# Optimization experiments

Hardware: AMD Instinct MI355X
Metric: run time of the kernel (lower is better)

The kernel has to match this reference:

```python
import jax, jax.numpy as jnp
import numpy as np

B, CL, QL, D = 32, 1024, 256, 768


def masked_softmax(x, m, axis):
    # Faithful port of the torch helper: clamp, pre-mask, stable exp, post-mask, eps-normalize.
    x = jnp.clip(x, -15.0, 15.0)
    x = x * m
    e_x = jnp.exp(x - jnp.max(x, axis=axis, keepdims=True))
    e_x = e_x * m
    return e_x / (jnp.sum(e_x, axis=axis, keepdims=True) + 1e-6)


def setup_inputs() -> dict:
    key = jax.random.key(0)
    k1, k2, k3, k4, k5 = jax.random.split(key, 5)
    C = jax.random.normal(k1, (B, CL, D), dtype=jnp.float32)
    Q = jax.random.normal(k2, (B, QL, D), dtype=jnp.float32)
    w = jax.random.normal(k3, (3 * D,), dtype=jnp.float32) * 0.02  # xavier-scale
    c_mask = jax.random.randint(k4, (B, CL), 0, 2, dtype=jnp.int32)
    q_mask = jax.random.randint(k5, (B, QL), 0, 2, dtype=jnp.int32)
    return {"C": C, "Q": Q, "w": w, "c_mask": c_mask, "q_mask": q_mask}


def reference(C, Q, w, c_mask, q_mask):
    d = C.shape[-1]
    w1, w2, w3 = w[:d], w[d:2 * d], w[2 * d:]
    # Trilinear decomposition of cat([C,Q,C*Q]) @ w -- same math, no [b,c,q,3d] blowup.
    S = (jnp.einsum('bid,d->bi', C, w1)[:, :, None]
         + jnp.einsum('bjd,d->bj', Q, w2)[:, None, :]
         + jnp.einsum('bid,bjd->bij', C * w3, Q))  # [B, CL, QL]
    qm = q_mask.astype(jnp.float32)[:, None, :]  # [B,1,QL]
    cm = c_mask.astype(jnp.float32)[:, :, None]  # [B,CL,1]
    S1 = masked_softmax(S, qm, axis=2)
    A = jnp.einsum('bij,bjd->bid', S1, Q)  # [B, CL, D]
    S2 = masked_softmax(S, cm, axis=1)
    S2_max = jnp.max(S2, axis=1, keepdims=True)  # [B, 1, QL]
    Bmat = jnp.einsum('bij,bjd->bid', S2_max, Q)  # [B, 1, D], broadcast over CL
    Bmat = jnp.broadcast_to(Bmat, C.shape)
    return jnp.concatenate([C, A, C * A, C * Bmat], axis=-1)  # [B, CL, 4D]
```

## Files before the change

### kernel.cpp

```cpp
#include <hip/hip_runtime.h>

#define B_  32
#define CL_ 1024
#define QL_ 256
#define D_  768

typedef _Float16 f16x8 __attribute__((ext_vector_type(8)));
typedef float    f32x4 __attribute__((ext_vector_type(4)));

__global__ void rowdot_kernel(const float* __restrict__ X, const float* __restrict__ w,
                              float* __restrict__ out) {
    int wave = threadIdx.x >> 6;
    int lane = threadIdx.x & 63;
    int row  = blockIdx.x * 4 + wave;
    const float* x = X + (size_t)row * D_;
    float s = 0.f;
#pragma unroll
    for (int k = 0; k < D_ / 64; ++k) s += x[lane + k * 64] * w[lane + k * 64];
#pragma unroll
    for (int m = 32; m; m >>= 1) s += __shfl_xor(s, m, 64);
    if (lane == 0) out[row] = s;
}

__global__ __launch_bounds__(256) void prep_q_kernel(const float* __restrict__ Q,
                                                     _Float16* __restrict__ QT,
                                                     _Float16* __restrict__ Qh) {
    __shared__ float tile[64][65];
    int b  = blockIdx.z;
    int j0 = blockIdx.x * 64;
    int d0 = blockIdx.y * 64;
    int t  = threadIdx.x;
    int jj = t >> 4;
    int dd = (t & 15) * 4;
#pragma unroll
    for (int p = 0; p < 4; ++p) {
        int j = jj + p * 16;
        f32x4 v = *(const f32x4*)(Q + ((size_t)b * QL_ + j0 + j) * D_ + d0 + dd);
        *(f32x4*)&tile[j][dd] = v;
        _Float16 h[4] = {(_Float16)v[0], (_Float16)v[1], (_Float16)v[2], (_Float16)v[3]};
        *(uint2*)(Qh + ((size_t)b * QL_ + j0 + j) * D_ + d0 + dd) = *(uint2*)h;
    }
    __syncthreads();
    int j4 = (t & 15) * 4;
#pragma unroll
    for (int p = 0; p < 4; ++p) {
        int d = jj + p * 16;
        _Float16 h[4];
#pragma unroll
        for (int e = 0; e < 4; ++e) h[e] = (_Float16)tile[j4 + e][d];
        *(uint2*)(QT + ((size_t)b * D_ + d0 + d) * QL_ + j0 + j4) = *(uint2*)h;
    }
}

__global__ __launch_bounds__(512, 2) void fused_s_kernel(
    const float* __restrict__ C, const _Float16* __restrict__ Qh,
    const float* __restrict__ w, const float* __restrict__ qw2g,
    const int* __restrict__ c_mask, const int* __restrict__ q_mask,
    _Float16* __restrict__ S1h, float* __restrict__ pmg,
    float* __restrict__ psg, float* __restrict__ pumg) {
    __shared__ __align__(16) _Float16 As[128 * 64];
    __shared__ __align__(16) _Float16 Bs[256 * 64];
    __shared__ float w1s[D_], w3s[D_];
    __shared__ float cw1s[128];
    __shared__ float rowredM[512], rowredS[512];
    __shared__ int   cms[128], qms[256];

    int t = threadIdx.x;
    int bid = blockIdx.x;
    int b = bid & 31;
    int slice = bid >> 5;
    int i0 = slice * 128;
    int wave = t >> 6, lane = t & 63, lrow = lane & 15, lk = lane >> 4;
    int wr = wave >> 2, wc = wave & 3;
    int jw = wc * 64;

    for (int k = t; k < D_; k += 512) { w1s[k] = w[k]; w3s[k] = w[2 * D_ + k]; }
    if (t < 128) cms[t] = c_mask[b * CL_ + i0 + t];
    if (t < 256) qms[t] = q_mask[b * QL_ + t];

    const float* Cbase = C + ((size_t)b * CL_ + i0) * D_;
    const _Float16* Qbase = Qh + (size_t)b * QL_ * D_;

    f32x4 acc[4][4] = {};
    float cwp0 = 0.f, cwp1 = 0.f;
    int arow0 = t >> 3, arow1 = 64 + (t >> 3);
    int asc = t & 7;

    for (int k0 = 0; k0 < D_; k0 += 64) {
        __syncthreads();
        {
            int kk0 = k0 + asc * 8;
            float4 w30 = *(const float4*)(&w3s[kk0]);
            float4 w31 = *(const float4*)(&w3s[kk0 + 4]);
            float4 w10 = *(const float4*)(&w1s[kk0]);
            float4 w11 = *(const float4*)(&w1s[kk0 + 4]);
            const float* src0 = Cbase + (size_t)arow0 * D_ + kk0;
            float4 a0 = *(const float4*)src0;
            float4 a1 = *(const float4*)(src0 + 4);
            f16x8 ah;
            ah[0] = (_Float16)(a0.x * w30.x); ah[1] = (_Float16)(a0.y * w30.y);
            ah[2] = (_Float16)(a0.z * w30.z); ah[3] = (_Float16)(a0.w * w30.w);
            ah[4] = (_Float16)(a1.x * w31.x); ah[5] = (_Float16)(a1.y * w31.y);
            ah[6] = (_Float16)(a1.z * w31.z); ah[7] = (_Float16)(a1.w * w31.w);
            cwp0 += a0.x * w10.x + a0.y * w10.y + a0.z * w10.z + a0.w * w10.w
                  + a1.x * w11.x + a1.y * w11.y + a1.z * w11.z + a1.w * w11.w;
            *(f16x8*)&As[arow0 * 64 + ((asc ^ (arow0 & 7)) * 8)] = ah;
            const float* src1 = Cbase + (size_t)arow1 * D_ + kk0;
            float4 b0 = *(const float4*)src1;
            float4 b1 = *(const float4*)(src1 + 4);
            f16x8 bh;
            bh[0] = (_Float16)(b0.x * w30.x); bh[1] = (_Float16)(b0.y * w30.y);
            bh[2] = (_Float16)(b0.z * w30.z); bh[3] = (_Float16)(b0.w * w30.w);
            bh[4] = (_Float16)(b1.x * w31.x); bh[5] = (_Float16)(b1.y * w31.y);
            bh[6] = (_Float16)(b1.z * w31.z); bh[7] = (_Float16)(b1.w * w31.w);
            cwp1 += b0.x * w10.x + b0.y * w10.y + b0.z * w10.z + b0.w * w10.w
                  + b1.x * w11.x + b1.y * w11.y + b1.z * w11.z + b1.w * w11.w;
            *(f16x8*)&As[arow1 * 64 + ((asc ^ (arow1 & 7)) * 8)] = bh;
        }
#pragma unroll
        for (int sb = 0; sb < 4; ++sb) {
            int row = sb * 64 + (t >> 3);
            f16x8 bh = *(const f16x8*)(Qbase + (size_t)row * D_ + k0 + asc * 8);
            *(f16x8*)&Bs[row * 64 + ((asc ^ (row & 7)) * 8)] = bh;
        }
        __syncthreads();
#pragma unroll
        for (int kk = 0; kk < 2; ++kk) {
            int slot = kk * 4 + lk;
            int swa = (slot ^ (lrow & 7)) * 8;
            f16x8 af[4];
#pragma unroll
            for (int m = 0; m < 4; ++m)
                af[m] = *(const f16x8*)&As[(wr * 64 + m * 16 + lrow) * 64 + swa];
#pragma unroll
            for (int n = 0; n < 4; ++n) {
                int rb = jw + n * 16 + lrow;
                f16x8 bf = *(const f16x8*)&Bs[rb * 64 + swa];
#pragma unroll
                for (int m = 0; m < 4; ++m)
                    acc[m][n] = __builtin_amdgcn_mfma_f32_16x16x32_f16(af[m], bf, acc[m][n], 0, 0, 0);
            }
        }
    }

    cwp0 += __shfl_xor(cwp0, 1, 64); cwp0 += __shfl_xor(cwp0, 2, 64); cwp0 += __shfl_xor(cwp0, 4, 64);
    cwp1 += __shfl_xor(cwp1, 1, 64); cwp1 += __shfl_xor(cwp1, 2, 64); cwp1 += __shfl_xor(cwp1, 4, 64);
    if ((t & 7) == 0) { cw1s[arow0] = cwp0; cw1s[arow1] = cwp1; }
    __syncthreads();

    float qwv[4]; int qmv[4];
#pragma unroll
    for (int n = 0; n < 4; ++n) {
        int j = jw + n * 16 + lrow;
        qwv[n] = qw2g[b * QL_ + j];
        qmv[n] = qms[j];
    }
#pragma unroll
    for (int m = 0; m < 4; ++m) {
#pragma unroll
        for (int r = 0; r < 4; ++r) {
            float cw = cw1s[wr * 64 + m * 16 + lk * 4 + r];
#pragma unroll
            for (int n = 0; n < 4; ++n) {
                float v = acc[m][n][r] + cw + qwv[n];
                acc[m][n][r] = fminf(15.f, fmaxf(-15.f, v));
            }
        }
    }

    {
        float pmv[4], psv[4], pumv[4];
#pragma unroll
        for (int n = 0; n < 4; ++n) {
            float pmax = -1e30f, umax = -1e30f;
#pragma unroll
            for (int m = 0; m < 4; ++m)
#pragma unroll
                for (int r = 0; r < 4; ++r) {
                    int cm = cms[wr * 64 + m * 16 + lk * 4 + r];
                    float v = acc[m][n][r];
                    pmax = fmaxf(pmax, cm ? v : 0.0f);
                    umax = fmaxf(umax, cm ? v : -1e30f);
                }
            float s = 0.f;
#pragma unroll
            for (int m = 0; m < 4; ++m)
#pragma unroll
                for (int r = 0; r < 4; ++r) {
                    int cm = cms[wr * 64 + m * 16 + lk * 4 + r];
                    s += cm ? __expf(acc[m][n][r] - pmax) : 0.0f;
                }
            pmv[n] = pmax; psv[n] = s; pumv[n] = umax;
        }
#pragma unroll
        for (int off = 16; off <= 32; off <<= 1) {
#pragma unroll
            for (int n = 0; n < 4; ++n) {
                float om = __shfl_xor(pmv[n], off, 64);
                float os = __shfl_xor(psv[n], off, 64);
                float ou = __shfl_xor(pumv[n], off, 64);
                float nm = fmaxf(pmv[n], om);
                psv[n] = psv[n] * __expf(pmv[n] - nm) + os * __expf(om - nm);
                pmv[n] = nm;
                pumv[n] = fmaxf(pumv[n], ou);
            }
        }
        if (lk == 0) {
#pragma unroll
            for (int n = 0; n < 4; ++n) {
                int idx = (b * 16 + slice * 2 + wr) * QL_ + jw + n * 16 + lrow;
                pmg[idx] = pmv[n]; psg[idx] = psv[n]; pumg[idx] = pumv[n];
            }
        }
    }

    float Mv[4][4];
#pragma unroll
    for (int m = 0; m < 4; ++m)
#pragma unroll
        for (int r = 0; r < 4; ++r) {
            float lm = qmv[0] ? acc[m][0][r] : 0.0f;
#pragma unroll
            for (int n = 1; n < 4; ++n) lm = fmaxf(lm, qmv[n] ? acc[m][n][r] : 0.0f);
            lm = fmaxf(lm, __shfl_xor(lm, 1, 64));
            lm = fmaxf(lm, __shfl_xor(lm, 2, 64));
            lm = fmaxf(lm, __shfl_xor(lm, 4, 64));
            lm = fmaxf(lm, __shfl_xor(lm, 8, 64));
            Mv[m][r] = lm;
        }
    if (lrow == 0) {
#pragma unroll
        for (int m = 0; m < 4; ++m)
#pragma unroll
            for (int r = 0; r < 4; ++r)
                rowredM[wave * 64 + m * 16 + lk * 4 + r] = Mv[m][r];
    }
    __syncthreads();
#pragma unroll
    for (int m = 0; m < 4; ++m)
#pragma unroll
        for (int r = 0; r < 4; ++r) {
            int row = wr * 256 + m * 16 + lk * 4 + r;
            Mv[m][r] = fmaxf(fmaxf(rowredM[row], rowredM[64 + row]),
                             fmaxf(rowredM[128 + row], rowredM[192 + row]));
        }
    float inv_[4][4];
#pragma unroll
    for (int m = 0; m < 4; ++m)
#pragma unroll
        for (int r = 0; r < 4; ++r) {
            float ls = 0.f;
#pragma unroll
            for (int n = 0; n < 4; ++n) {
                float e = qmv[n] ? __expf(acc[m][n][r] - Mv[m][r]) : 0.0f;
                acc[m][n][r] = e;
                ls += e;
            }
            ls += __shfl_xor(ls, 1, 64);
            ls += __shfl_xor(ls, 2, 64);
            ls += __shfl_xor(ls, 4, 64);
            ls += __shfl_xor(ls, 8, 64);
            if (lrow == 0) rowredS[wave * 64 + m * 16 + lk * 4 + r] = ls;
        }
    __syncthreads();
#pragma unroll
    for (int m = 0; m < 4; ++m)
#pragma unroll
        for (int r = 0; r < 4; ++r) {
            int row = wr * 256 + m * 16 + lk * 4 + r;
            float sum = rowredS[row] + rowredS[64 + row] + rowredS[128 + row] + rowredS[192 + row];
            inv_[m][r] = 1.0f / (sum + 1e-6f);
        }

    char* Bs2 = (char*)Bs;
#pragma unroll
    for (int p = 0; p < 2; ++p) {
        __syncthreads();
        if (wr == p) {
#pragma unroll
            for (int m = 0; m < 4; ++m)
#pragma unroll
                for (int n = 0; n < 4; ++n)
#pragma unroll
                    for (int r = 0; r < 4; ++r) {
                        int il = m * 16 + lk * 4 + r;
                        int jj = jw + n * 16 + lrow;
                        int byte = il * 512 + (((jj >> 3) ^ (il & 7)) * 16) + (jj & 7) * 2;
                        *(_Float16*)(Bs2 + byte) = (_Float16)(acc[m][n][r] * inv_[m][r]);
                    }
        }
        __syncthreads();
#pragma unroll
        for (int sb = 0; sb < 4; ++sb) {
            int row = sb * 16 + (t >> 5);
            int c = t & 31;
            uint4 v = *(uint4*)(Bs2 + row * 512 + ((c ^ (row & 7)) * 16));
            *(uint4*)(S1h + ((size_t)(b * CL_ + i0 + p * 64 + row)) * QL_ + c * 8) = v;
        }
    }
}

__global__ void combine_bmat_kernel(const float* __restrict__ pm, const float* __restrict__ ps,
                                    const float* __restrict__ pum, const _Float16* __restrict__ Qh,
                                    float* __restrict__ bmat) {
    __shared__ float sm[QL_];
    int b = blockIdx.x;
    int t = threadIdx.x;
    {
        float m = -1e30f, s = 0.f, um = -1e30f;
        for (int k = 0; k < 16; ++k) {
            int idx = (b * 16 + k) * QL_ + t;
            float mk = pm[idx], sk = ps[idx], umk = pum[idx];
            float nm = fmaxf(m, mk);
            s = s * __expf(m - nm) + sk * __expf(mk - nm);
            m = nm;
            um = fmaxf(um, umk);
        }
        sm[t] = (um < -1e29f) ? 0.0f : __expf(um - m) / (s + 1e-6f);
    }
    __syncthreads();
#pragma unroll
    for (int c = 0; c < 3; ++c) {
        int d = c * 256 + t;
        const _Float16* qb = Qh + (size_t)b * QL_ * D_ + d;
        float s = 0.f;
        for (int j = 0; j < QL_; ++j) s += sm[j] * (float)qb[(size_t)j * D_];
        bmat[b * D_ + d] = s;
    }
}

__global__ __launch_bounds__(512) void agemm_out_kernel(
    const _Float16* __restrict__ S1h, const _Float16* __restrict__ QTh,
    const float* __restrict__ C, const float* __restrict__ bmat, float* __restrict__ out) {
    __shared__ __align__(16) _Float16 As[128 * 64];
    __shared__ __align__(16) _Float16 Bs[128 * 64];
    __shared__ __align__(16) float fbuf[64 * 132];
    int t  = threadIdx.x;
    int bid = blockIdx.x;
    int b = bid & 31;
    int tile = bid >> 5;
    int d0 = (tile % 6) * 128;
    int i0 = (tile / 6) * 128;
    const _Float16* Sbase = S1h + ((size_t)b * CL_ + i0) * QL_;
    const _Float16* Qbase = QTh + ((size_t)b * D_ + d0) * QL_;
    int wave = t >> 6, lane = t & 63, lrow = lane & 15, lk = lane >> 4;
    int wr = wave >> 1, wc = wave & 1;
    f32x4 acc[2][4] = {};
    int srow = t >> 3, sc = t & 7;
    for (int k0 = 0; k0 < QL_; k0 += 64) {
        __syncthreads();
#pragma unroll
        for (int s2 = 0; s2 < 2; ++s2) {
            int row = s2 * 64 + srow;
            int sw = (sc ^ (row & 7)) * 8;
            f16x8 av = *(const f16x8*)(Sbase + (size_t)row * QL_ + k0 + sc * 8);
            f16x8 bv = *(const f16x8*)(Qbase + (size_t)row * QL_ + k0 + sc * 8);
            *(f16x8*)&As[row * 64 + sw] = av;
            *(f16x8*)&Bs[row * 64 + sw] = bv;
        }
        __syncthreads();
#pragma unroll
        for (int kk = 0; kk < 2; ++kk) {
            int slot = kk * 4 + lk;
            int swa = (slot ^ (lrow & 7)) * 8;
            f16x8 qf[2];
#pragma unroll
            for (int m = 0; m < 2; ++m)
                qf[m] = *(const f16x8*)&Bs[(wr * 32 + m * 16 + lrow) * 64 + swa];
#pragma unroll
            for (int n = 0; n < 4; ++n) {
                f16x8 sf = *(const f16x8*)&As[(wc * 64 + n * 16 + lrow) * 64 + swa];
#pragma unroll
                for (int m = 0; m < 2; ++m)
                    acc[m][n] = __builtin_amdgcn_mfma_f32_16x16x32_f16(qf[m], sf, acc[m][n], 0, 0, 0);
            }
        }
    }
    int c32 = t & 31;
    f32x4 bm4 = *(const f32x4*)(bmat + b * D_ + d0 + c32 * 4);
#pragma unroll
    for (int p = 0; p < 2; ++p) {
        if (wc == p) {
#pragma unroll
            for (int n = 0; n < 4; ++n)
#pragma unroll
                for (int m = 0; m < 2; ++m)
                    *(f32x4*)&fbuf[(n * 16 + lrow) * 132 + wr * 32 + m * 16 + lk * 4] = acc[m][n];
        }
        __syncthreads();
#pragma unroll
        for (int q = 0; q < 4; ++q) {
            int row = q * 16 + (t >> 5);
            int i = i0 + p * 64 + row;
            f32x4 a4 = *(const f32x4*)&fbuf[row * 132 + c32 * 4];
            f32x4 c4 = *(const f32x4*)(C + ((size_t)b * CL_ + i) * D_ + d0 + c32 * 4);
            size_t ob = ((size_t)b * CL_ + i) * (size_t)(4 * D_) + d0 + c32 * 4;
            __builtin_nontemporal_store(c4,       (f32x4*)(out + ob));
            __builtin_nontemporal_store(a4,       (f32x4*)(out + ob + D_));
            __builtin_nontemporal_store(c4 * a4,  (f32x4*)(out + ob + 2 * D_));
            __builtin_nontemporal_store(c4 * bm4, (f32x4*)(out + ob + 3 * D_));
        }
        if (p == 0) __syncthreads();
    }
}

extern "C" void kernel_launch(void* const* d_in, const int* in_sizes, int n_in,
                              void* d_out, int out_size, void* d_ws, size_t ws_size,
                              hipStream_t stream) {
    const float* C      = (const float*)d_in[0];
    const float* Q      = (const float*)d_in[1];
    const float* w      = (const float*)d_in[2];
    const int*   c_mask = (const int*)d_in[3];
    const int*   q_mask = (const int*)d_in[4];
    float* out = (float*)d_out;
    char* ws = (char*)d_ws;

    _Float16* S1h   = (_Float16*)(ws);
    _Float16* QTh   = (_Float16*)(ws + 16777216);
    _Float16* Qh    = (_Float16*)(ws + 29360128);
    float*    qw2   = (float*)(ws + 41943040);
    float*    pm    = (float*)(ws + 41975808);
    float*    ps    = (float*)(ws + 42500096);
    float*    pum   = (float*)(ws + 43024384);
    float*    bmat  = (float*)(ws + 43581440);

    rowdot_kernel<<<dim3((B_ * QL_) / 4), 256, 0, stream>>>(Q, w + D_, qw2);
    prep_q_kernel<<<dim3(QL_ / 64, D_ / 64, B_), 256, 0, stream>>>(Q, QTh, Qh);
    fused_s_kernel<<<dim3(256), 512, 0, stream>>>(C, Qh, w, qw2, c_mask, q_mask,
                                                  S1h, pm, ps, pum);
    combine_bmat_kernel<<<dim3(B_), 256, 0, stream>>>(pm, ps, pum, Qh, bmat);
    agemm_out_kernel<<<dim3(1536), 512, 0, stream>>>(S1h, QTh, C, bmat, out);
}
```

Baseline: 177.7 us.

## Fuse score, bmat combine and output GEMM into one kernel with grid barrier

Merges the score/softmax kernel, the bmat combine kernel and the A-GEMM/output kernel into a single persistent kernel. S1 stays in LDS instead of being written to and reread from global memory, and slice-0 blocks compute bmat after spinning on a global atomic counter. The other blocks wait on a second counter before the epilogue. This removes two launches and the S1 round trip, but it relies on all 256 blocks being co-resident for the spin barriers and cuts the output-phase grid from 1536 blocks to 256, which may reduce parallelism and latency hiding.

```diff
diff --git a/kernel.cpp b/kernel.cpp
--- a/kernel.cpp
+++ b/kernel.cpp
@@ -52,17 +52,21 @@
     }
 }
 
-__global__ __launch_bounds__(512, 2) void fused_s_kernel(
+__global__ __launch_bounds__(512, 2) void fused_all_kernel(
     const float* __restrict__ C, const _Float16* __restrict__ Qh,
+    const _Float16* __restrict__ QTh,
     const float* __restrict__ w, const float* __restrict__ qw2g,
     const int* __restrict__ c_mask, const int* __restrict__ q_mask,
-    _Float16* __restrict__ S1h, float* __restrict__ pmg,
-    float* __restrict__ psg, float* __restrict__ pumg) {
-    __shared__ __align__(16) _Float16 As[128 * 64];
-    __shared__ __align__(16) _Float16 Bs[256 * 64];
+    float* __restrict__ pmg, float* __restrict__ psg, float* __restrict__ pumg,
+    float* __restrict__ bmat_g, int* __restrict__ bar, float* __restrict__ out) {
+
+    __shared__ __align__(16) char  S1b[128 * 512];
+    __shared__ __align__(16) char  blob[50176];
     __shared__ float w1s[D_], w3s[D_];
     __shared__ float cw1s[128];
     __shared__ float rowredM[512], rowredS[512];
+    __shared__ float sm2[QL_];
+    __shared__ float bmat_lds[D_];
     __shared__ int   cms[128], qms[256];
 
     int t = threadIdx.x;
@@ -74,12 +78,16 @@
     int wr = wave >> 2, wc = wave & 3;
     int jw = wc * 64;
 
+    _Float16* As = (_Float16*)blob;
+    _Float16* Bs = (_Float16*)(blob + 16384);
+
     for (int k = t; k < D_; k += 512) { w1s[k] = w[k]; w3s[k] = w[2 * D_ + k]; }
     if (t < 128) cms[t] = c_mask[b * CL_ + i0 + t];
     if (t < 256) qms[t] = q_mask[b * QL_ + t];
 
     const float* Cbase = C + ((size_t)b * CL_ + i0) * D_;
     const _Float16* Qbase = Qh + (size_t)b * QL_ * D_;
+    const _Float16* QTbase = QTh + (size_t)b * D_ * QL_;
 
     f32x4 acc[4][4] = {};
     float cwp0 = 0.f, cwp1 = 0.f;
@@ -134,8 +142,7 @@
                 af[m] = *(const f16x8*)&As[(wr * 64 + m * 16 + lrow) * 64 + swa];
 #pragma unroll
             for (int n = 0; n < 4; ++n) {
-                int rb = jw + n * 16 + lrow;
-                f16x8 bf = *(const f16x8*)&Bs[rb * 64 + swa];
+                f16x8 bf = *(const f16x8*)&Bs[(jw + n * 16 + lrow) * 64 + swa];
 #pragma unroll
                 for (int m = 0; m < 4; ++m)
                     acc[m][n] = __builtin_amdgcn_mfma_f32_16x16x32_f16(af[m], bf, acc[m][n], 0, 0, 0);
@@ -213,6 +220,9 @@
             }
         }
     }
+    __threadfence();
+    __syncthreads();
+    if (t == 0) atomicAdd(&bar[0], 1);
 
     float Mv[4][4];
 #pragma unroll
@@ -271,136 +281,122 @@
             float sum = rowredS[row] + rowredS[64 + row] + rowredS[128 + row] + rowredS[192 + row];
             inv_[m][r] = 1.0f / (sum + 1e-6f);
         }
-
-    char* Bs2 = (char*)Bs;
-#pragma unroll
-    for (int p = 0; p < 2; ++p) {
+#pragma unroll
+    for (int m = 0; m < 4; ++m)
+#pragma unroll
+        for (int n = 0; n < 4; ++n)
+#pragma unroll
+            for (int r = 0; r < 4; ++r) {
+                int il = wr * 64 + m * 16 + lk * 4 + r;
+                int jj = jw + n * 16 + lrow;
+                int byte = il * 512 + (((jj >> 3) ^ (il & 7)) * 16) + (jj & 7) * 2;
+                *(_Float16*)(S1b + byte) = (_Float16)(acc[m][n][r] * inv_[m][r]);
+            }
+
+    if (slice == 0) {
+        if (t == 0) { while (atomicAdd(&bar[0], 0) < 256) __builtin_amdgcn_s_sleep(2); }
         __syncthreads();
-        if (wr == p) {
-#pragma unroll
-            for (int m = 0; m < 4; ++m)
+        __threadfence();
+        if (t < QL_) {
+            float m = -1e30f, s = 0.f, um = -1e30f;
+            for (int k = 0; k < 16; ++k) {
+                int idx = (b * 16 + k) * QL_ + t;
+                float mk  = atomicAdd(&pmg[idx], 0.0f);
+                float sk  = atomicAdd(&psg[idx], 0.0f);
+                float umk = atomicAdd(&pumg[idx], 0.0f);
+                float nm = fmaxf(m, mk);
+                s = s * __expf(m - nm) + sk * __expf(mk - nm);
+                m = nm;
+                um = fmaxf(um, umk);
+            }
+            sm2[t] = (um < -1e29f) ? 0.0f : __expf(um - m) / (s + 1e-6f);
+        }
+        __syncthreads();
+        for (int d = t; d < D_; d += 512) {
+            const _Float16* qt = QTbase + (size_t)d * QL_;
+            float s = 0.f;
+            for (int j8 = 0; j8 < QL_; j8 += 8) {
+                f16x8 v = *(const f16x8*)(qt + j8);
+#pragma unroll
+                for (int e = 0; e < 8; ++e) s += sm2[j8 + e] * (float)v[e];
+            }
+            bmat_g[b * D_ + d] = s;
+        }
+        __threadfence();
+        __syncthreads();
+        if (t == 0) atomicAdd(&bar[1], 1);
+    }
+
+    _Float16* QTs = (_Float16*)blob;
+    float* fbuf = (float*)(blob + 16384);
+    int wr2 = wave >> 2, wc2 = wave & 3;
+    int c32 = t & 31;
+
+    for (int dt = 0; dt < 6; ++dt) {
+        int d0g = dt * 128;
+        f32x4 acc2[2][4] = {};
+        for (int j0 = 0; j0 < QL_; j0 += 64) {
+            __syncthreads();
+#pragma unroll
+            for (int s2 = 0; s2 < 2; ++s2) {
+                int slot = t * 2 + s2;
+                int row = slot >> 3, sc = slot & 7;
+                f16x8 v = *(const f16x8*)(QTbase + (size_t)(d0g + row) * QL_ + j0 + sc * 8);
+                *(f16x8*)&QTs[row * 64 + ((sc ^ (row & 7)) * 8)] = v;
+            }
+            __syncthreads();
+#pragma unroll
+            for (int kk = 0; kk < 2; ++kk) {
+                int slot = kk * 4 + lk;
+                f16x8 qf[2];
+#pragma unroll
+                for (int m = 0; m < 2; ++m) {
+                    int rd = wc2 * 32 + m * 16 + lrow;
+                    qf[m] = *(const f16x8*)&QTs[rd * 64 + ((slot ^ (rd & 7)) * 8)];
+                }
+                int u = (j0 >> 3) + kk * 4 + lk;
+#pragma unroll
+                for (int n = 0; n < 4; ++n) {
+                    int il = wr2 * 64 + n * 16 + lrow;
+                    f16x8 sf = *(const f16x8*)(S1b + il * 512 + ((u ^ (il & 7)) * 16));
+#pragma unroll
+                    for (int m = 0; m < 2; ++m)
+                        acc2[m][n] = __builtin_amdgcn_mfma_f32_16x16x32_f16(qf[m], sf, acc2[m][n], 0, 0, 0);
+                }
+            }
+        }
+        if (dt == 0) {
+            if (t == 0) { while (atomicAdd(&bar[1], 0) < 32) __builtin_amdgcn_s_sleep(2); }
+            __syncthreads();
+            __threadfence();
+            for (int idx = t; idx < D_; idx += 512)
+                bmat_lds[idx] = atomicAdd(&bmat_g[b * D_ + idx], 0.0f);
+        }
+#pragma unroll
+        for (int p = 0; p < 2; ++p) {
+            __syncthreads();
+            if (wr2 == p) {
 #pragma unroll
                 for (int n = 0; n < 4; ++n)
 #pragma unroll
-                    for (int r = 0; r < 4; ++r) {
-                        int il = m * 16 + lk * 4 + r;
-                        int jj = jw + n * 16 + lrow;
-                        int byte = il * 512 + (((jj >> 3) ^ (il & 7)) * 16) + (jj & 7) * 2;
-                        *(_Float16*)(Bs2 + byte) = (_Float16)(acc[m][n][r] * inv_[m][r]);
-                    }
-        }
-        __syncthreads();
-#pragma unroll
-        for (int sb = 0; sb < 4; ++sb) {
-            int row = sb * 16 + (t >> 5);
-            int c = t & 31;
-            uint4 v = *(uint4*)(Bs2 + row * 512 + ((c ^ (row & 7)) * 16));
-            *(uint4*)(S1h + ((size_t)(b * CL_ + i0 + p * 64 + row)) * QL_ + c * 8) = v;
-        }
-    }
-}
-
-__global__ void combine_bmat_kernel(const float* __restrict__ pm, const float* __restrict__ ps,
-                                    const float* __restrict__ pum, const _Float16* __restrict__ Qh,
-                                    float* __restrict__ bmat) {
-    __shared__ float sm[QL_];
-    int b = blockIdx.x;
-    int t = threadIdx.x;
-    {
-        float m = -1e30f, s = 0.f, um = -1e30f;
-        for (int k = 0; k < 16; ++k) {
-            int idx = (b * 16 + k) * QL_ + t;
-            float mk = pm[idx], sk = ps[idx], umk = pum[idx];
-            float nm = fmaxf(m, mk);
-            s = s * __expf(m - nm) + sk * __expf(mk - nm);
-            m = nm;
-            um = fmaxf(um, umk);
-        }
-        sm[t] = (um < -1e29f) ? 0.0f : __expf(um - m) / (s + 1e-6f);
-    }
-    __syncthreads();
-#pragma unroll
-    for (int c = 0; c < 3; ++c) {
-        int d = c * 256 + t;
-        const _Float16* qb = Qh + (size_t)b * QL_ * D_ + d;
-        float s = 0.f;
-        for (int j = 0; j < QL_; ++j) s += sm[j] * (float)qb[(size_t)j * D_];
-        bmat[b * D_ + d] = s;
-    }
-}
-
-__global__ __launch_bounds__(512) void agemm_out_kernel(
-    const _Float16* __restrict__ S1h, const _Float16* __restrict__ QTh,
-    const float* __restrict__ C, const float* __restrict__ bmat, float* __restrict__ out) {
-    __shared__ __align__(16) _Float16 As[128 * 64];
-    __shared__ __align__(16) _Float16 Bs[128 * 64];
-    __shared__ __align__(16) float fbuf[64 * 132];
-    int t  = threadIdx.x;
-    int bid = blockIdx.x;
-    int b = bid & 31;
-    int tile = bid >> 5;
-    int d0 = (tile % 6) * 128;
-    int i0 = (tile / 6) * 128;
-    const _Float16* Sbase = S1h + ((size_t)b * CL_ + i0) * QL_;
-    const _Float16* Qbase = QTh + ((size_t)b * D_ + d0) * QL_;
-    int wave = t >> 6, lane = t & 63, lrow = lane & 15, lk = lane >> 4;
-    int wr = wave >> 1, wc = wave & 1;
-    f32x4 acc[2][4] = {};
-    int srow = t >> 3, sc = t & 7;
-    for (int k0 = 0; k0 < QL_; k0 += 64) {
-        __syncthreads();
-#pragma unroll
-        for (int s2 = 0; s2 < 2; ++s2) {
-            int row = s2 * 64 + srow;
-            int sw = (sc ^ (row & 7)) * 8;
-            f16x8 av = *(const f16x8*)(Sbase + (size_t)row * QL_ + k0 + sc * 8);
-            f16x8 bv = *(const f16x8*)(Qbase + (size_t)row * QL_ + k0 + sc * 8);
-            *(f16x8*)&As[row * 64 + sw] = av;
-            *(f16x8*)&Bs[row * 64 + sw] = bv;
-        }
-        __syncthreads();
-#pragma unroll
-        for (int kk = 0; kk < 2; ++kk) {
-            int slot = kk * 4 + lk;
-            int swa = (slot ^ (lrow & 7)) * 8;
-            f16x8 qf[2];
-#pragma unroll
-            for (int m = 0; m < 2; ++m)
-                qf[m] = *(const f16x8*)&Bs[(wr * 32 + m * 16 + lrow) * 64 + swa];
-#pragma unroll
-            for (int n = 0; n < 4; ++n) {
-                f16x8 sf = *(const f16x8*)&As[(wc * 64 + n * 16 + lrow) * 64 + swa];
-#pragma unroll
-                for (int m = 0; m < 2; ++m)
-                    acc[m][n] = __builtin_amdgcn_mfma_f32_16x16x32_f16(qf[m], sf, acc[m][n], 0, 0, 0);
-            }
-        }
-    }
-    int c32 = t & 31;
-    f32x4 bm4 = *(const f32x4*)(bmat + b * D_ + d0 + c32 * 4);
-#pragma unroll
-    for (int p = 0; p < 2; ++p) {
-        if (wc == p) {
-#pragma unroll
-            for (int n = 0; n < 4; ++n)
-#pragma unroll
-                for (int m = 0; m < 2; ++m)
-                    *(f32x4*)&fbuf[(n * 16 + lrow) * 132 + wr * 32 + m * 16 + lk * 4] = acc[m][n];
-        }
-        __syncthreads();
-#pragma unroll
-        for (int q = 0; q < 4; ++q) {
-            int row = q * 16 + (t >> 5);
-            int i = i0 + p * 64 + row;
-            f32x4 a4 = *(const f32x4*)&fbuf[row * 132 + c32 * 4];
-            f32x4 c4 = *(const f32x4*)(C + ((size_t)b * CL_ + i) * D_ + d0 + c32 * 4);
-            size_t ob = ((size_t)b * CL_ + i) * (size_t)(4 * D_) + d0 + c32 * 4;
-            __builtin_nontemporal_store(c4,       (f32x4*)(out + ob));
-            __builtin_nontemporal_store(a4,       (f32x4*)(out + ob + D_));
-            __builtin_nontemporal_store(c4 * a4,  (f32x4*)(out + ob + 2 * D_));
-            __builtin_nontemporal_store(c4 * bm4, (f32x4*)(out + ob + 3 * D_));
-        }
-        if (p == 0) __syncthreads();
+                    for (int m = 0; m < 2; ++m)
+                        *(f32x4*)&fbuf[(n * 16 + lrow) * 132 + wc2 * 32 + m * 16 + lk * 4] = acc2[m][n];
+            }
+            __syncthreads();
+            f32x4 bm4 = *(const f32x4*)&bmat_lds[d0g + c32 * 4];
+#pragma unroll
+            for (int q = 0; q < 4; ++q) {
+                int row = q * 16 + (t >> 5);
+                int i = i0 + p * 64 + row;
+                f32x4 a4 = *(const f32x4*)&fbuf[row * 132 + c32 * 4];
+                f32x4 c4 = *(const f32x4*)(C + ((size_t)b * CL_ + i) * D_ + d0g + c32 * 4);
+                size_t ob = ((size_t)b * CL_ + i) * (size_t)(4 * D_) + d0g + c32 * 4;
+                __builtin_nontemporal_store(c4,       (f32x4*)(out + ob));
+                __builtin_nontemporal_store(a4,       (f32x4*)(out + ob + D_));
+                __builtin_nontemporal_store(c4 * a4,  (f32x4*)(out + ob + 2 * D_));
+                __builtin_nontemporal_store(c4 * bm4, (f32x4*)(out + ob + 3 * D_));
+            }
+        }
     }
 }
 
@@ -415,19 +411,18 @@
     float* out = (float*)d_out;
     char* ws = (char*)d_ws;
 
-    _Float16* S1h   = (_Float16*)(ws);
-    _Float16* QTh   = (_Float16*)(ws + 16777216);
-    _Float16* Qh    = (_Float16*)(ws + 29360128);
-    float*    qw2   = (float*)(ws + 41943040);
-    float*    pm    = (float*)(ws + 41975808);
-    float*    ps    = (float*)(ws + 42500096);
-    float*    pum   = (float*)(ws + 43024384);
-    float*    bmat  = (float*)(ws + 43581440);
-
+    _Float16* QTh   = (_Float16*)(ws);
+    _Float16* Qh    = (_Float16*)(ws + 12582912);
+    float*    qw2   = (float*)(ws + 25165824);
+    float*    pm    = (float*)(ws + 25198592);
+    float*    ps    = (float*)(ws + 25722880);
+    float*    pum   = (float*)(ws + 26247168);
+    float*    bmat  = (float*)(ws + 26771456);
+    int*      bar   = (int*)(ws + 26869760);
+
+    hipMemsetAsync(bar, 0, 64, stream);
     rowdot_kernel<<<dim3((B_ * QL_) / 4), 256, 0, stream>>>(Q, w + D_, qw2);
     prep_q_kernel<<<dim3(QL_ / 64, D_ / 64, B_), 256, 0, stream>>>(Q, QTh, Qh);
-    fused_s_kernel<<<dim3(256), 512, 0, stream>>>(C, Qh, w, qw2, c_mask, q_mask,
-                                                  S1h, pm, ps, pum);
-    combine_bmat_kernel<<<dim3(B_), 256, 0, stream>>>(pm, ps, pum, Qh, bmat);
-    agemm_out_kernel<<<dim3(1536), 512, 0, stream>>>(S1h, QTh, C, bmat, out);
+    fused_all_kernel<<<dim3(256), 512, 0, stream>>>(C, Qh, QTh, w, qw2, c_mask, q_mask,
+                                                    pm, ps, pum, bmat, bar, out);
 }
```

New measurement: 235.2 us. 1.32x slower.

## Fuse row-dot into Q prep and Bmat combine into S kernel tail

Applied to the files above, without the earlier changes.

The Q·w2 row-dot is now computed inside prep_q_kernel while Q is being loaded and transposed. That kernel is restructured so each block loops over all of D for 32 rows. The separate combine_bmat kernel is removed. The last fused_s block per batch, found through an atomic counter, now merges the softmax partials and computes Bmat from the transposed Q. This cuts two kernel launches and a pass over Q, but adds a memset, a serialized tail in 32 blocks, and atomic-based cross-block ordering.

```diff
diff --git a/kernel.cpp b/kernel.cpp
--- a/kernel.cpp
+++ b/kernel.cpp
@@ -8,62 +8,62 @@
 typedef _Float16 f16x8 __attribute__((ext_vector_type(8)));
 typedef float    f32x4 __attribute__((ext_vector_type(4)));
 
-__global__ void rowdot_kernel(const float* __restrict__ X, const float* __restrict__ w,
-                              float* __restrict__ out) {
-    int wave = threadIdx.x >> 6;
-    int lane = threadIdx.x & 63;
-    int row  = blockIdx.x * 4 + wave;
-    const float* x = X + (size_t)row * D_;
-    float s = 0.f;
-#pragma unroll
-    for (int k = 0; k < D_ / 64; ++k) s += x[lane + k * 64] * w[lane + k * 64];
-#pragma unroll
-    for (int m = 32; m; m >>= 1) s += __shfl_xor(s, m, 64);
-    if (lane == 0) out[row] = s;
-}
-
 __global__ __launch_bounds__(256) void prep_q_kernel(const float* __restrict__ Q,
+                                                     const float* __restrict__ w,
                                                      _Float16* __restrict__ QT,
-                                                     _Float16* __restrict__ Qh) {
-    __shared__ float tile[64][65];
-    int b  = blockIdx.z;
-    int j0 = blockIdx.x * 64;
-    int d0 = blockIdx.y * 64;
+                                                     _Float16* __restrict__ Qh,
+                                                     float* __restrict__ qw2) {
+    __shared__ float tile[32][73];
+    int b  = blockIdx.y;
+    int j0 = blockIdx.x * 32;
     int t  = threadIdx.x;
-    int jj = t >> 4;
-    int dd = (t & 15) * 4;
-#pragma unroll
-    for (int p = 0; p < 4; ++p) {
-        int j = jj + p * 16;
-        f32x4 v = *(const f32x4*)(Q + ((size_t)b * QL_ + j0 + j) * D_ + d0 + dd);
-        *(f32x4*)&tile[j][dd] = v;
-        _Float16 h[4] = {(_Float16)v[0], (_Float16)v[1], (_Float16)v[2], (_Float16)v[3]};
-        *(uint2*)(Qh + ((size_t)b * QL_ + j0 + j) * D_ + d0 + dd) = *(uint2*)h;
-    }
-    __syncthreads();
-    int j4 = (t & 15) * 4;
-#pragma unroll
-    for (int p = 0; p < 4; ++p) {
-        int d = jj + p * 16;
-        _Float16 h[4];
-#pragma unroll
-        for (int e = 0; e < 4; ++e) h[e] = (_Float16)tile[j4 + e][d];
-        *(uint2*)(QT + ((size_t)b * D_ + d0 + d) * QL_ + j0 + j4) = *(uint2*)h;
-    }
+    int jj = t >> 3;
+    int dd = (t & 7) * 8;
+    int dT = t >> 2;
+    int j8 = (t & 3) * 8;
+    float part = 0.f;
+    for (int c = 0; c < 12; ++c) {
+        int d0 = c * 64;
+        const float* src = Q + ((size_t)b * QL_ + j0 + jj) * D_ + d0 + dd;
+        float4 v0 = *(const float4*)src;
+        float4 v1 = *(const float4*)(src + 4);
+        *(float4*)&tile[jj][dd]     = v0;
+        *(float4*)&tile[jj][dd + 4] = v1;
+        _Float16 h[8] = {(_Float16)v0.x, (_Float16)v0.y, (_Float16)v0.z, (_Float16)v0.w,
+                         (_Float16)v1.x, (_Float16)v1.y, (_Float16)v1.z, (_Float16)v1.w};
+        *(uint4*)(Qh + ((size_t)b * QL_ + j0 + jj) * D_ + d0 + dd) = *(uint4*)h;
+        float4 w0 = *(const float4*)(w + D_ + d0 + dd);
+        float4 w1 = *(const float4*)(w + D_ + d0 + dd + 4);
+        part += v0.x * w0.x + v0.y * w0.y + v0.z * w0.z + v0.w * w0.w
+              + v1.x * w1.x + v1.y * w1.y + v1.z * w1.z + v1.w * w1.w;
+        __syncthreads();
+        _Float16 g[8];
+#pragma unroll
+        for (int e = 0; e < 8; ++e) g[e] = (_Float16)tile[j8 + e][dT];
+        *(uint4*)(QT + ((size_t)b * D_ + d0 + dT) * QL_ + j0 + j8) = *(uint4*)g;
+        __syncthreads();
+    }
+    part += __shfl_xor(part, 1, 64);
+    part += __shfl_xor(part, 2, 64);
+    part += __shfl_xor(part, 4, 64);
+    if ((t & 7) == 0) qw2[b * QL_ + j0 + jj] = part;
 }
 
 __global__ __launch_bounds__(512, 2) void fused_s_kernel(
     const float* __restrict__ C, const _Float16* __restrict__ Qh,
+    const _Float16* __restrict__ QTh,
     const float* __restrict__ w, const float* __restrict__ qw2g,
     const int* __restrict__ c_mask, const int* __restrict__ q_mask,
     _Float16* __restrict__ S1h, float* __restrict__ pmg,
-    float* __restrict__ psg, float* __restrict__ pumg) {
+    float* __restrict__ psg, float* __restrict__ pumg,
+    float* __restrict__ bmat_g, int* __restrict__ cnt) {
     __shared__ __align__(16) _Float16 As[128 * 64];
     __shared__ __align__(16) _Float16 Bs[256 * 64];
     __shared__ float w1s[D_], w3s[D_];
     __shared__ float cw1s[128];
     __shared__ float rowredM[512], rowredS[512];
     __shared__ int   cms[128], qms[256];
+    __shared__ int   lastFlag;
 
     int t = threadIdx.x;
     int bid = blockIdx.x;
@@ -134,8 +134,7 @@
                 af[m] = *(const f16x8*)&As[(wr * 64 + m * 16 + lrow) * 64 + swa];
 #pragma unroll
             for (int n = 0; n < 4; ++n) {
-                int rb = jw + n * 16 + lrow;
-                f16x8 bf = *(const f16x8*)&Bs[rb * 64 + swa];
+                f16x8 bf = *(const f16x8*)&Bs[(jw + n * 16 + lrow) * 64 + swa];
 #pragma unroll
                 for (int m = 0; m < 4; ++m)
                     acc[m][n] = __builtin_amdgcn_mfma_f32_16x16x32_f16(af[m], bf, acc[m][n], 0, 0, 0);
@@ -298,34 +297,52 @@
             *(uint4*)(S1h + ((size_t)(b * CL_ + i0 + p * 64 + row)) * QL_ + c * 8) = v;
         }
     }
-}
-
-__global__ void combine_bmat_kernel(const float* __restrict__ pm, const float* __restrict__ ps,
-                                    const float* __restrict__ pum, const _Float16* __restrict__ Qh,
-                                    float* __restrict__ bmat) {
-    __shared__ float sm[QL_];
-    int b = blockIdx.x;
-    int t = threadIdx.x;
-    {
+
+    __threadfence();
+    __syncthreads();
+    if (t == 0) lastFlag = (atomicAdd(&cnt[b], 1) == 7);
+    __syncthreads();
+    if (lastFlag) {
+        __threadfence();
+        float* cmb  = (float*)As;
+        float* sm2p = cmb + 1536;
+        int j = t & 255, half = t >> 8;
         float m = -1e30f, s = 0.f, um = -1e30f;
-        for (int k = 0; k < 16; ++k) {
-            int idx = (b * 16 + k) * QL_ + t;
-            float mk = pm[idx], sk = ps[idx], umk = pum[idx];
+        for (int k = half * 8; k < half * 8 + 8; ++k) {
+            int idx = (b * 16 + k) * QL_ + j;
+            float mk  = atomicAdd(&pmg[idx], 0.0f);
+            float sk  = atomicAdd(&psg[idx], 0.0f);
+            float umk = atomicAdd(&pumg[idx], 0.0f);
             float nm = fmaxf(m, mk);
             s = s * __expf(m - nm) + sk * __expf(mk - nm);
             m = nm;
             um = fmaxf(um, umk);
         }
-        sm[t] = (um < -1e29f) ? 0.0f : __expf(um - m) / (s + 1e-6f);
-    }
-    __syncthreads();
-#pragma unroll
-    for (int c = 0; c < 3; ++c) {
-        int d = c * 256 + t;
-        const _Float16* qb = Qh + (size_t)b * QL_ * D_ + d;
-        float s = 0.f;
-        for (int j = 0; j < QL_; ++j) s += sm[j] * (float)qb[(size_t)j * D_];
-        bmat[b * D_ + d] = s;
+        cmb[half * 256 + j] = m;
+        cmb[512 + half * 256 + j] = s;
+        cmb[1024 + half * 256 + j] = um;
+        __syncthreads();
+        if (t < 256) {
+            float m0 = cmb[t], m1 = cmb[256 + t];
+            float s0 = cmb[512 + t], s1 = cmb[768 + t];
+            float u0 = cmb[1024 + t], u1 = cmb[1280 + t];
+            float nm = fmaxf(m0, m1);
+            float ss = s0 * __expf(m0 - nm) + s1 * __expf(m1 - nm);
+            float uu = fmaxf(u0, u1);
+            sm2p[t] = (uu < -1e29f) ? 0.0f : __expf(uu - nm) / (ss + 1e-6f);
+        }
+        __syncthreads();
+        const _Float16* QTbase = QTh + (size_t)b * D_ * QL_;
+        for (int d = t; d < D_; d += 512) {
+            const _Float16* qt = QTbase + (size_t)d * QL_;
+            float s2 = 0.f;
+            for (int j8 = 0; j8 < QL_; j8 += 8) {
+                f16x8 v = *(const f16x8*)(qt + j8);
+#pragma unroll
+                for (int e = 0; e < 8; ++e) s2 += sm2p[j8 + e] * (float)v[e];
+            }
+            bmat_g[b * D_ + d] = s2;
+        }
     }
 }
 
@@ -423,11 +440,11 @@
     float*    ps    = (float*)(ws + 42500096);
     float*    pum   = (float*)(ws + 43024384);
     float*    bmat  = (float*)(ws + 43581440);
-
-    rowdot_kernel<<<dim3((B_ * QL_) / 4), 256, 0, stream>>>(Q, w + D_, qw2);
-    prep_q_kernel<<<dim3(QL_ / 64, D_ / 64, B_), 256, 0, stream>>>(Q, QTh, Qh);
-    fused_s_kernel<<<dim3(256), 512, 0, stream>>>(C, Qh, w, qw2, c_mask, q_mask,
-                                                  S1h, pm, ps, pum);
-    combine_bmat_kernel<<<dim3(B_), 256, 0, stream>>>(pm, ps, pum, Qh, bmat);
+    int*      cnt   = (int*)(ws + 43679744);
+
+    hipMemsetAsync(cnt, 0, 128, stream);
+    prep_q_kernel<<<dim3(QL_ / 32, B_), 256, 0, stream>>>(Q, w, QTh, Qh, qw2);
+    fused_s_kernel<<<dim3(256), 512, 0, stream>>>(C, Qh, QTh, w, qw2, c_mask, q_mask,
+                                                  S1h, pm, ps, pum, bmat, cnt);
     agemm_out_kernel<<<dim3(1536), 512, 0, stream>>>(S1h, QTh, C, bmat, out);
 }
```

Result: slower. 217.9 us (+22.6%).

## Fuse Q·w2 rowdot into Q prep and Bmat combine into output GEMM

Applied to the files above, without the earlier changes.

The Q·w2 row dot product moves into prep_q_kernel as shuffle-reduced partials plus atomicAdd into a zeroed buffer, which removes a separate pass over Q. The combine_bmat kernel is folded into agemm_out_kernel: the tile-0 block of each batch computes the column-softmax max and Bmat, then publishes a release flag. The other blocks spin on that flag before their epilogue. This cuts two launches and a serial kernel boundary, but it relies on the tile-0 blocks being scheduled and making progress, and it adds float atomics that make the sum order nondeterministic.

```diff
diff --git a/kernel.cpp b/kernel.cpp
--- a/kernel.cpp
+++ b/kernel.cpp
@@ -8,30 +8,27 @@
 typedef _Float16 f16x8 __attribute__((ext_vector_type(8)));
 typedef float    f32x4 __attribute__((ext_vector_type(4)));
 
-__global__ void rowdot_kernel(const float* __restrict__ X, const float* __restrict__ w,
-                              float* __restrict__ out) {
-    int wave = threadIdx.x >> 6;
-    int lane = threadIdx.x & 63;
-    int row  = blockIdx.x * 4 + wave;
-    const float* x = X + (size_t)row * D_;
-    float s = 0.f;
-#pragma unroll
-    for (int k = 0; k < D_ / 64; ++k) s += x[lane + k * 64] * w[lane + k * 64];
-#pragma unroll
-    for (int m = 32; m; m >>= 1) s += __shfl_xor(s, m, 64);
-    if (lane == 0) out[row] = s;
+__global__ void zero_kernel(float* __restrict__ qw2, int* __restrict__ flag) {
+    int idx = blockIdx.x * 256 + threadIdx.x;
+    qw2[idx] = 0.f;
+    if (idx < 32) flag[idx] = 0;
 }
 
 __global__ __launch_bounds__(256) void prep_q_kernel(const float* __restrict__ Q,
+                                                     const float* __restrict__ w,
                                                      _Float16* __restrict__ QT,
-                                                     _Float16* __restrict__ Qh) {
+                                                     _Float16* __restrict__ Qh,
+                                                     float* __restrict__ qw2) {
     __shared__ float tile[64][65];
     int b  = blockIdx.z;
     int j0 = blockIdx.x * 64;
     int d0 = blockIdx.y * 64;
     int t  = threadIdx.x;
+    int lane = t & 63;
     int jj = t >> 4;
     int dd = (t & 15) * 4;
+    float4 wv = *(const float4*)(w + D_ + d0 + dd);
+    float part[4];
 #pragma unroll
     for (int p = 0; p < 4; ++p) {
         int j = jj + p * 16;
@@ -39,6 +36,7 @@
         *(f32x4*)&tile[j][dd] = v;
         _Float16 h[4] = {(_Float16)v[0], (_Float16)v[1], (_Float16)v[2], (_Float16)v[3]};
         *(uint2*)(Qh + ((size_t)b * QL_ + j0 + j) * D_ + d0 + dd) = *(uint2*)h;
+        part[p] = v[0] * wv.x + v[1] * wv.y + v[2] * wv.z + v[3] * wv.w;
     }
     __syncthreads();
     int j4 = (t & 15) * 4;
@@ -49,6 +47,14 @@
 #pragma unroll
         for (int e = 0; e < 4; ++e) h[e] = (_Float16)tile[j4 + e][d];
         *(uint2*)(QT + ((size_t)b * D_ + d0 + d) * QL_ + j0 + j4) = *(uint2*)h;
+    }
+#pragma unroll
+    for (int p = 0; p < 4; ++p) {
+        part[p] += __shfl_xor(part[p], 1, 64);
+        part[p] += __shfl_xor(part[p], 2, 64);
+        part[p] += __shfl_xor(part[p], 4, 64);
+        part[p] += __shfl_xor(part[p], 8, 64);
+        if ((lane & 15) == 0) atomicAdd(&qw2[b * QL_ + j0 + jj + p * 16], part[p]);
     }
 }
 
@@ -134,8 +140,7 @@
                 af[m] = *(const f16x8*)&As[(wr * 64 + m * 16 + lrow) * 64 + swa];
 #pragma unroll
             for (int n = 0; n < 4; ++n) {
-                int rb = jw + n * 16 + lrow;
-                f16x8 bf = *(const f16x8*)&Bs[rb * 64 + swa];
+                f16x8 bf = *(const f16x8*)&Bs[(jw + n * 16 + lrow) * 64 + swa];
 #pragma unroll
                 for (int m = 0; m < 4; ++m)
                     acc[m][n] = __builtin_amdgcn_mfma_f32_16x16x32_f16(af[m], bf, acc[m][n], 0, 0, 0);
@@ -300,38 +305,12 @@
     }
 }
 
-__global__ void combine_bmat_kernel(const float* __restrict__ pm, const float* __restrict__ ps,
-                                    const float* __restrict__ pum, const _Float16* __restrict__ Qh,
-                                    float* __restrict__ bmat) {
-    __shared__ float sm[QL_];
-    int b = blockIdx.x;
-    int t = threadIdx.x;
-    {
-        float m = -1e30f, s = 0.f, um = -1e30f;
-        for (int k = 0; k < 16; ++k) {
-            int idx = (b * 16 + k) * QL_ + t;
-            float mk = pm[idx], sk = ps[idx], umk = pum[idx];
-            float nm = fmaxf(m, mk);
-            s = s * __expf(m - nm) + sk * __expf(mk - nm);
-            m = nm;
-            um = fmaxf(um, umk);
-        }
-        sm[t] = (um < -1e29f) ? 0.0f : __expf(um - m) / (s + 1e-6f);
-    }
-    __syncthreads();
-#pragma unroll
-    for (int c = 0; c < 3; ++c) {
-        int d = c * 256 + t;
-        const _Float16* qb = Qh + (size_t)b * QL_ * D_ + d;
-        float s = 0.f;
-        for (int j = 0; j < QL_; ++j) s += sm[j] * (float)qb[(size_t)j * D_];
-        bmat[b * D_ + d] = s;
-    }
-}
-
 __global__ __launch_bounds__(512) void agemm_out_kernel(
     const _Float16* __restrict__ S1h, const _Float16* __restrict__ QTh,
-    const float* __restrict__ C, const float* __restrict__ bmat, float* __restrict__ out) {
+    const float* __restrict__ C,
+    const float* __restrict__ pmg, const float* __restrict__ psg,
+    const float* __restrict__ pumg,
+    float* __restrict__ bmat, int* __restrict__ flag, float* __restrict__ out) {
     __shared__ __align__(16) _Float16 As[128 * 64];
     __shared__ __align__(16) _Float16 Bs[128 * 64];
     __shared__ __align__(16) float fbuf[64 * 132];
@@ -341,6 +320,52 @@
     int tile = bid >> 5;
     int d0 = (tile % 6) * 128;
     int i0 = (tile / 6) * 128;
+
+    if (tile == 0) {
+        float* cmb  = fbuf;
+        float* sm2p = fbuf + 1536;
+        int j = t & 255, half = t >> 8;
+        float m = -1e30f, s = 0.f, um = -1e30f;
+        for (int k = half * 8; k < half * 8 + 8; ++k) {
+            int idx = (b * 16 + k) * QL_ + j;
+            float mk = pmg[idx], sk = psg[idx], umk = pumg[idx];
+            float nm = fmaxf(m, mk);
+            s = s * __expf(m - nm) + sk * __expf(mk - nm);
+            m = nm;
+            um = fmaxf(um, umk);
+        }
+        cmb[half * 256 + j] = m;
+        cmb[512 + half * 256 + j] = s;
+        cmb[1024 + half * 256 + j] = um;
+        __syncthreads();
+        if (t < 256) {
+            float m0 = cmb[t], m1 = cmb[256 + t];
+            float s0 = cmb[512 + t], s1 = cmb[768 + t];
+            float u0 = cmb[1024 + t], u1 = cmb[1280 + t];
+            float nm = fmaxf(m0, m1);
+            float ss = s0 * __expf(m0 - nm) + s1 * __expf(m1 - nm);
+            float uu = fmaxf(u0, u1);
+            sm2p[t] = (uu < -1e29f) ? 0.0f : __expf(uu - nm) / (ss + 1e-6f);
+        }
+        __syncthreads();
+        const _Float16* QTb = QTh + (size_t)b * D_ * QL_;
+        for (int d = t; d < D_; d += 512) {
+            const _Float16* qt = QTb + (size_t)d * QL_;
+            float s2 = 0.f;
+            for (int j8 = 0; j8 < QL_; j8 += 8) {
+                f16x8 v = *(const f16x8*)(qt + j8);
+#pragma unroll
+                for (int e = 0; e < 8; ++e) s2 += sm2p[j8 + e] * (float)v[e];
+            }
+            bmat[b * D_ + d] = s2;
+        }
+        __threadfence();
+        __syncthreads();
+        if (t == 0)
+            __hip_atomic_store(&flag[b], 1, __ATOMIC_RELEASE, __HIP_MEMORY_SCOPE_AGENT);
+        __syncthreads();
+    }
+
     const _Float16* Sbase = S1h + ((size_t)b * CL_ + i0) * QL_;
     const _Float16* Qbase = QTh + ((size_t)b * D_ + d0) * QL_;
     int wave = t >> 6, lane = t & 63, lrow = lane & 15, lk = lane >> 4;
@@ -376,10 +401,23 @@
             }
         }
     }
+
+    if (t == 0) {
+        while (__hip_atomic_load(&flag[b], __ATOMIC_ACQUIRE, __HIP_MEMORY_SCOPE_AGENT) == 0)
+            __builtin_amdgcn_s_sleep(2);
+    }
+    __syncthreads();
     int c32 = t & 31;
-    f32x4 bm4 = *(const f32x4*)(bmat + b * D_ + d0 + c32 * 4);
+    float bmv[4];
+#pragma unroll
+    for (int e = 0; e < 4; ++e)
+        bmv[e] = __hip_atomic_load(&bmat[b * D_ + d0 + c32 * 4 + e],
+                                   __ATOMIC_RELAXED, __HIP_MEMORY_SCOPE_AGENT);
+    f32x4 bm4 = {bmv[0], bmv[1], bmv[2], bmv[3]};
+
 #pragma unroll
     for (int p = 0; p < 2; ++p) {
+        __syncthreads();
         if (wc == p) {
 #pragma unroll
             for (int n = 0; n < 4; ++n)
@@ -400,7 +438,6 @@
             __builtin_nontemporal_store(c4 * a4,  (f32x4*)(out + ob + 2 * D_));
             __builtin_nontemporal_store(c4 * bm4, (f32x4*)(out + ob + 3 * D_));
         }
-        if (p == 0) __syncthreads();
     }
 }
 
@@ -423,11 +460,12 @@
     float*    ps    = (float*)(ws + 42500096);
     float*    pum   = (float*)(ws + 43024384);
     float*    bmat  = (float*)(ws + 43581440);
-
-    rowdot_kernel<<<dim3((B_ * QL_) / 4), 256, 0, stream>>>(Q, w + D_, qw2);
-    prep_q_kernel<<<dim3(QL_ / 64, D_ / 64, B_), 256, 0, stream>>>(Q, QTh, Qh);
+    int*      flag  = (int*)(ws + 43679744);
+
+    zero_kernel<<<dim3(32), 256, 0, stream>>>(qw2, flag);
+    prep_q_kernel<<<dim3(QL_ / 64, D_ / 64, B_), 256, 0, stream>>>(Q, w, QTh, Qh, qw2);
     fused_s_kernel<<<dim3(256), 512, 0, stream>>>(C, Qh, w, qw2, c_mask, q_mask,
                                                   S1h, pm, ps, pum);
-    combine_bmat_kernel<<<dim3(B_), 256, 0, stream>>>(pm, ps, pum, Qh, bmat);
-    agemm_out_kernel<<<dim3(1536), 512, 0, stream>>>(S1h, QTh, C, bmat, out);
+    agemm_out_kernel<<<dim3(1536), 512, 0, stream>>>(S1h, QTh, C, pm, ps, pum,
+                                                     bmat, flag, out);
 }
```

After: 318.3 us. 1.79x slower.
